# Kernel optimization log

Measured on AMD Instinct MI355X. Metric: run time of the kernel, lower is better.

## Reference

```python
import jax, jax.numpy as jnp
import numpy as np
import math

B, H, S, D = 256, 32, 16, 64
SCALE = 1.0 / math.sqrt(8.0)  # module hardcodes sqrt(8)
DROP_P = 0.3


def setup_inputs() -> dict:
    key = jax.random.key(0)
    kq, kk, kv = jax.random.split(key, 3)
    q = jax.random.normal(kq, (B, H, S, D), dtype=jnp.float32)
    k = jax.random.normal(kk, (B, H, S, D), dtype=jnp.float32)
    v = jax.random.normal(kv, (B, H, S, D), dtype=jnp.float32)
    return {"q": q, "k": k, "v": v}


def reference(q, k, v):
    # attn = (q @ k^T) / sqrt(8) + ones(16,16)
    attn = jnp.einsum("bhsd,bhtd->bhst", q, k) * SCALE
    attn = attn + jnp.ones((S, S), dtype=attn.dtype)  # additive mask (all ones)
    attn = jax.nn.softmax(attn, axis=-1)
    # dropout p=0.3 (training mode), fixed key for reproducibility
    keep = jax.random.bernoulli(jax.random.key(42), 1.0 - DROP_P, attn.shape)
    attn = jnp.where(keep, attn / (1.0 - DROP_P), 0.0)
    return jnp.einsum("bhst,bhtd->bhsd", attn, v)
```

## Files before the change

kernel.cpp:

```cpp
#include <hip/hip_runtime.h>
#include <hip/hip_bf16.h>
#include <stdint.h>
#include <stddef.h>


typedef __attribute__((ext_vector_type(8))) short short8;
typedef __attribute__((ext_vector_type(4))) float f32x4;
typedef __attribute__((ext_vector_type(4))) unsigned int u32x4;

#define VST 68
#define PST 24

__device__ __forceinline__ unsigned pk2_bf16(float a, float b) {
  float2 t; t.x = a; t.y = b;
  __hip_bfloat162 h = __float22bfloat162_rn(t);
  unsigned r;
  __builtin_memcpy(&r, &h, 4);
  return r;
}

__device__ __forceinline__ unsigned threefry_bits(unsigned idx) {
  const unsigned k0 = 0u, k1 = 42u;
  const unsigned k2 = k0 ^ k1 ^ 0x1BD11BDAu;
  unsigned x0 = k0;
  unsigned x1 = idx + k1;
#define TF_ROUND(r) { x0 += x1; x1 = (x1 << (r)) | (x1 >> (32 - (r))); x1 ^= x0; }
  TF_ROUND(13) TF_ROUND(15) TF_ROUND(26) TF_ROUND(6)
  x0 += k1; x1 += k2 + 1u;
  TF_ROUND(17) TF_ROUND(29) TF_ROUND(16) TF_ROUND(24)
  x0 += k2; x1 += k0 + 2u;
  TF_ROUND(13) TF_ROUND(15) TF_ROUND(26) TF_ROUND(6)
  x0 += k0; x1 += k1 + 3u;
  TF_ROUND(17) TF_ROUND(29) TF_ROUND(16) TF_ROUND(24)
  x0 += k1; x1 += k2 + 4u;
  TF_ROUND(13) TF_ROUND(15) TF_ROUND(26) TF_ROUND(6)
  x0 += k2; x1 += k0 + 5u;
#undef TF_ROUND
  return x0 ^ x1;
}

__device__ __forceinline__ void drop_mask(int bh, int base, float* m) {
#pragma unroll
  for (int t = 0; t < 4; t++) {
    unsigned idx = ((unsigned)bh << 8) + (unsigned)(base + t);
    unsigned bits = threefry_bits(idx);
    float u = __builtin_bit_cast(float, 0x3F800000u | (bits >> 9)) - 1.0f;
    m[t] = (u < 0.7f) ? (1.0f / 0.7f) : 0.0f;
  }
}

__device__ __forceinline__ void cvt_hilo_f4(float4 a, float4 b, short8& hi, short8& lo) {
  float x[8] = {a.x, a.y, a.z, a.w, b.x, b.y, b.z, b.w};
  u32x4 hw, lw;
#pragma unroll
  for (int i = 0; i < 4; i++) {
    float e0 = x[2 * i], e1 = x[2 * i + 1];
    unsigned hp = pk2_bf16(e0, e1);
    float h0 = __builtin_bit_cast(float, hp << 16);
    float h1 = __builtin_bit_cast(float, hp & 0xFFFF0000u);
    unsigned lp = pk2_bf16(e0 - h0, e1 - h1);
    hw[i] = hp; lw[i] = lp;
  }
  hi = __builtin_bit_cast(short8, hw);
  lo = __builtin_bit_cast(short8, lw);
}

__global__ __launch_bounds__(256, 8) void attn_kernel(
    const float* __restrict__ q, const float* __restrict__ k,
    const float* __restrict__ v, float* __restrict__ out) {
  __shared__ __align__(16) unsigned short vst[4][16 * VST];
  __shared__ __align__(16) unsigned short pst[4][16 * PST];

  const int lane = threadIdx.x & 63;
  const int w = threadIdx.x >> 6;
  const int bh = blockIdx.x * 4 + w;
  const int c = lane & 15;
  const int g = lane >> 4;

  const float4* qr = (const float4*)(q + (size_t)bh * 1024 + c * 64 + g * 8);
  const float4* kr = (const float4*)(k + (size_t)bh * 1024 + c * 64 + g * 8);
  float4 qv0 = qr[0], qv1 = qr[1], qv2 = qr[8], qv3 = qr[9];
  float4 kv0 = kr[0], kv1 = kr[1], kv2 = kr[8], kv3 = kr[9];
  const float4* vs = (const float4*)(v + (size_t)bh * 1024);
  float4 vt0 = vs[lane], vt1 = vs[64 + lane], vt2 = vs[128 + lane], vt3 = vs[192 + lane];

  float m[4];
  drop_mask(bh, (c << 4) + 4 * g, m);

  short8 qhi0, qlo0, qhi1, qlo1, khi0, klo0, khi1, klo1;
  cvt_hilo_f4(qv0, qv1, qhi0, qlo0);
  cvt_hilo_f4(qv2, qv3, qhi1, qlo1);
  cvt_hilo_f4(kv0, kv1, khi0, klo0);
  cvt_hilo_f4(kv2, kv3, khi1, klo1);

  f32x4 acc = {0.f, 0.f, 0.f, 0.f};
  acc = __builtin_amdgcn_mfma_f32_16x16x32_bf16(khi0, qhi0, acc, 0, 0, 0);
  acc = __builtin_amdgcn_mfma_f32_16x16x32_bf16(khi1, qhi1, acc, 0, 0, 0);
  acc = __builtin_amdgcn_mfma_f32_16x16x32_bf16(klo0, qhi0, acc, 0, 0, 0);
  acc = __builtin_amdgcn_mfma_f32_16x16x32_bf16(klo1, qhi1, acc, 0, 0, 0);
  acc = __builtin_amdgcn_mfma_f32_16x16x32_bf16(khi0, qlo0, acc, 0, 0, 0);
  acc = __builtin_amdgcn_mfma_f32_16x16x32_bf16(khi1, qlo1, acc, 0, 0, 0);

  const float SCALE = 0.35355339059327373f;
  float sv[4];
#pragma unroll
  for (int t = 0; t < 4; t++) sv[t] = acc[t] * SCALE;
  float mx = fmaxf(fmaxf(sv[0], sv[1]), fmaxf(sv[2], sv[3]));
  mx = fmaxf(mx, __shfl_xor(mx, 16));
  mx = fmaxf(mx, __shfl_xor(mx, 32));
  float p0 = __expf(sv[0] - mx), p1 = __expf(sv[1] - mx);
  float p2v = __expf(sv[2] - mx), p3 = __expf(sv[3] - mx);
  float sum = (p0 + p1) + (p2v + p3);
  sum += __shfl_xor(sum, 16);
  sum += __shfl_xor(sum, 32);
  float rs = 1.0f / sum;
  float ad[4] = {p0 * rs * m[0], p1 * rs * m[1], p2v * rs * m[2], p3 * rs * m[3]};

  unsigned short* vw = &vst[w][0];
  {
    float4 vv;
    unsigned w0, w1;
    vv = vt0; w0 = pk2_bf16(vv.x, vv.y); w1 = pk2_bf16(vv.z, vv.w);
    *(uint2*)(&vw[(0 + g) * VST + 4 * c]) = make_uint2(w0, w1);
    vv = vt1; w0 = pk2_bf16(vv.x, vv.y); w1 = pk2_bf16(vv.z, vv.w);
    *(uint2*)(&vw[(4 + g) * VST + 4 * c]) = make_uint2(w0, w1);
    vv = vt2; w0 = pk2_bf16(vv.x, vv.y); w1 = pk2_bf16(vv.z, vv.w);
    *(uint2*)(&vw[(8 + g) * VST + 4 * c]) = make_uint2(w0, w1);
    vv = vt3; w0 = pk2_bf16(vv.x, vv.y); w1 = pk2_bf16(vv.z, vv.w);
    *(uint2*)(&vw[(12 + g) * VST + 4 * c]) = make_uint2(w0, w1);
  }

  unsigned short* pw = &pst[w][0];
  {
    unsigned w0 = pk2_bf16(ad[0], ad[1]), w1 = pk2_bf16(ad[2], ad[3]);
    *(uint2*)(&pw[c * PST + 4 * g]) = make_uint2(w0, w1);
  }

  short8 pa = {0, 0, 0, 0, 0, 0, 0, 0};
  if (g < 2) pa = *(const short8*)(&pw[c * PST + g * 8]);

  f32x4 oacc[4];
#pragma unroll
  for (int nt = 0; nt < 4; nt++) {
    short8 vb = {0, 0, 0, 0, 0, 0, 0, 0};
    if (g < 2) {
#pragma unroll
      for (int j = 0; j < 8; j++)
        vb[j] = (short)vw[(g * 8 + j) * VST + nt * 16 + c];
    }
    f32x4 z = {0.f, 0.f, 0.f, 0.f};
    oacc[nt] = __builtin_amdgcn_mfma_f32_16x16x32_bf16(pa, vb, z, 0, 0, 0);
  }

  float* op = out + (size_t)bh * 1024;
#pragma unroll
  for (int nt = 0; nt < 4; nt++)
#pragma unroll
    for (int t = 0; t < 4; t++)
      op[(4 * g + t) * 64 + nt * 16 + c] = oacc[nt][t];
}

extern "C" void kernel_launch(void* const* d_in, const int* in_sizes, int n_in,
                              void* d_out, int out_size, void* d_ws, size_t ws_size,
                              hipStream_t stream) {
  const float* q = (const float*)d_in[0];
  const float* k = (const float*)d_in[1];
  const float* v = (const float*)d_in[2];
  float* out = (float*)d_out;
  attn_kernel<<<2048, 256, 0, stream>>>(q, k, v, out);
}
```

Before: 136.5 us.

## Process four heads per wave with register double-buffered prefetch

Each wave now loops over four consecutive batch-heads. It loads the next head's q, k, v and computes its dropout mask while working on the current head. The grid shrinks to a quarter of the blocks, and launch bounds are relaxed to allow more registers. This aims to hide global load latency through explicit prefetch, at the cost of fewer resident waves and more register pressure.

```diff
diff --git a/kernel.cpp b/kernel.cpp
--- a/kernel.cpp
+++ b/kernel.cpp
@@ -65,7 +65,7 @@
   lo = __builtin_bit_cast(short8, lw);
 }
 
-__global__ __launch_bounds__(256, 8) void attn_kernel(
+__global__ __launch_bounds__(256, 2) void attn_kernel(
     const float* __restrict__ q, const float* __restrict__ k,
     const float* __restrict__ v, float* __restrict__ out) {
   __shared__ __align__(16) unsigned short vst[4][16 * VST];
@@ -73,91 +73,115 @@
 
   const int lane = threadIdx.x & 63;
   const int w = threadIdx.x >> 6;
-  const int bh = blockIdx.x * 4 + w;
+  const int base = (blockIdx.x * 4 + w) * 4;
   const int c = lane & 15;
   const int g = lane >> 4;
 
-  const float4* qr = (const float4*)(q + (size_t)bh * 1024 + c * 64 + g * 8);
-  const float4* kr = (const float4*)(k + (size_t)bh * 1024 + c * 64 + g * 8);
-  float4 qv0 = qr[0], qv1 = qr[1], qv2 = qr[8], qv3 = qr[9];
-  float4 kv0 = kr[0], kv1 = kr[1], kv2 = kr[8], kv3 = kr[9];
-  const float4* vs = (const float4*)(v + (size_t)bh * 1024);
-  float4 vt0 = vs[lane], vt1 = vs[64 + lane], vt2 = vs[128 + lane], vt3 = vs[192 + lane];
+  float4 qv[2][4], kv[2][4], vt[2][4];
+  float m[2][4];
 
-  float m[4];
-  drop_mask(bh, (c << 4) + 4 * g, m);
-
-  short8 qhi0, qlo0, qhi1, qlo1, khi0, klo0, khi1, klo1;
-  cvt_hilo_f4(qv0, qv1, qhi0, qlo0);
-  cvt_hilo_f4(qv2, qv3, qhi1, qlo1);
-  cvt_hilo_f4(kv0, kv1, khi0, klo0);
-  cvt_hilo_f4(kv2, kv3, khi1, klo1);
-
-  f32x4 acc = {0.f, 0.f, 0.f, 0.f};
-  acc = __builtin_amdgcn_mfma_f32_16x16x32_bf16(khi0, qhi0, acc, 0, 0, 0);
-  acc = __builtin_amdgcn_mfma_f32_16x16x32_bf16(khi1, qhi1, acc, 0, 0, 0);
-  acc = __builtin_amdgcn_mfma_f32_16x16x32_bf16(klo0, qhi0, acc, 0, 0, 0);
-  acc = __builtin_amdgcn_mfma_f32_16x16x32_bf16(klo1, qhi1, acc, 0, 0, 0);
-  acc = __builtin_amdgcn_mfma_f32_16x16x32_bf16(khi0, qlo0, acc, 0, 0, 0);
-  acc = __builtin_amdgcn_mfma_f32_16x16x32_bf16(khi1, qlo1, acc, 0, 0, 0);
-
-  const float SCALE = 0.35355339059327373f;
-  float sv[4];
-#pragma unroll
-  for (int t = 0; t < 4; t++) sv[t] = acc[t] * SCALE;
-  float mx = fmaxf(fmaxf(sv[0], sv[1]), fmaxf(sv[2], sv[3]));
-  mx = fmaxf(mx, __shfl_xor(mx, 16));
-  mx = fmaxf(mx, __shfl_xor(mx, 32));
-  float p0 = __expf(sv[0] - mx), p1 = __expf(sv[1] - mx);
-  float p2v = __expf(sv[2] - mx), p3 = __expf(sv[3] - mx);
-  float sum = (p0 + p1) + (p2v + p3);
-  sum += __shfl_xor(sum, 16);
-  sum += __shfl_xor(sum, 32);
-  float rs = 1.0f / sum;
-  float ad[4] = {p0 * rs * m[0], p1 * rs * m[1], p2v * rs * m[2], p3 * rs * m[3]};
+  {
+    const float4* qr = (const float4*)(q + (size_t)base * 1024 + c * 64 + g * 8);
+    const float4* kr = (const float4*)(k + (size_t)base * 1024 + c * 64 + g * 8);
+    qv[0][0] = qr[0]; qv[0][1] = qr[1]; qv[0][2] = qr[8]; qv[0][3] = qr[9];
+    kv[0][0] = kr[0]; kv[0][1] = kr[1]; kv[0][2] = kr[8]; kv[0][3] = kr[9];
+    const float4* vs = (const float4*)(v + (size_t)base * 1024);
+    vt[0][0] = vs[lane]; vt[0][1] = vs[64 + lane];
+    vt[0][2] = vs[128 + lane]; vt[0][3] = vs[192 + lane];
+    drop_mask(base, (c << 4) + 4 * g, m[0]);
+  }
 
   unsigned short* vw = &vst[w][0];
-  {
-    float4 vv;
-    unsigned w0, w1;
-    vv = vt0; w0 = pk2_bf16(vv.x, vv.y); w1 = pk2_bf16(vv.z, vv.w);
-    *(uint2*)(&vw[(0 + g) * VST + 4 * c]) = make_uint2(w0, w1);
-    vv = vt1; w0 = pk2_bf16(vv.x, vv.y); w1 = pk2_bf16(vv.z, vv.w);
-    *(uint2*)(&vw[(4 + g) * VST + 4 * c]) = make_uint2(w0, w1);
-    vv = vt2; w0 = pk2_bf16(vv.x, vv.y); w1 = pk2_bf16(vv.z, vv.w);
-    *(uint2*)(&vw[(8 + g) * VST + 4 * c]) = make_uint2(w0, w1);
-    vv = vt3; w0 = pk2_bf16(vv.x, vv.y); w1 = pk2_bf16(vv.z, vv.w);
-    *(uint2*)(&vw[(12 + g) * VST + 4 * c]) = make_uint2(w0, w1);
+  unsigned short* pw = &pst[w][0];
+
+#pragma unroll
+  for (int h = 0; h < 4; h++) {
+    const int b = h & 1, nb = b ^ 1;
+    const int bh = base + h;
+
+    if (h < 3) {
+      const int bhn = bh + 1;
+      const float4* qr = (const float4*)(q + (size_t)bhn * 1024 + c * 64 + g * 8);
+      const float4* kr = (const float4*)(k + (size_t)bhn * 1024 + c * 64 + g * 8);
+      qv[nb][0] = qr[0]; qv[nb][1] = qr[1]; qv[nb][2] = qr[8]; qv[nb][3] = qr[9];
+      kv[nb][0] = kr[0]; kv[nb][1] = kr[1]; kv[nb][2] = kr[8]; kv[nb][3] = kr[9];
+      const float4* vs = (const float4*)(v + (size_t)bhn * 1024);
+      vt[nb][0] = vs[lane]; vt[nb][1] = vs[64 + lane];
+      vt[nb][2] = vs[128 + lane]; vt[nb][3] = vs[192 + lane];
+      drop_mask(bhn, (c << 4) + 4 * g, m[nb]);
+    }
+
+    short8 qhi0, qlo0, qhi1, qlo1, khi0, klo0, khi1, klo1;
+    cvt_hilo_f4(qv[b][0], qv[b][1], qhi0, qlo0);
+    cvt_hilo_f4(qv[b][2], qv[b][3], qhi1, qlo1);
+    cvt_hilo_f4(kv[b][0], kv[b][1], khi0, klo0);
+    cvt_hilo_f4(kv[b][2], kv[b][3], khi1, klo1);
+
+    f32x4 acc = {0.f, 0.f, 0.f, 0.f};
+    acc = __builtin_amdgcn_mfma_f32_16x16x32_bf16(khi0, qhi0, acc, 0, 0, 0);
+    acc = __builtin_amdgcn_mfma_f32_16x16x32_bf16(khi1, qhi1, acc, 0, 0, 0);
+    acc = __builtin_amdgcn_mfma_f32_16x16x32_bf16(klo0, qhi0, acc, 0, 0, 0);
+    acc = __builtin_amdgcn_mfma_f32_16x16x32_bf16(klo1, qhi1, acc, 0, 0, 0);
+    acc = __builtin_amdgcn_mfma_f32_16x16x32_bf16(khi0, qlo0, acc, 0, 0, 0);
+    acc = __builtin_amdgcn_mfma_f32_16x16x32_bf16(khi1, qlo1, acc, 0, 0, 0);
+
+    const float SCALE = 0.35355339059327373f;
+    float sv[4];
+#pragma unroll
+    for (int t = 0; t < 4; t++) sv[t] = acc[t] * SCALE;
+    float mx = fmaxf(fmaxf(sv[0], sv[1]), fmaxf(sv[2], sv[3]));
+    mx = fmaxf(mx, __shfl_xor(mx, 16));
+    mx = fmaxf(mx, __shfl_xor(mx, 32));
+    float p0 = __expf(sv[0] - mx), p1 = __expf(sv[1] - mx);
+    float p2v = __expf(sv[2] - mx), p3 = __expf(sv[3] - mx);
+    float sum = (p0 + p1) + (p2v + p3);
+    sum += __shfl_xor(sum, 16);
+    sum += __shfl_xor(sum, 32);
+    float rs = 1.0f / sum;
+    float ad[4] = {p0 * rs * m[b][0], p1 * rs * m[b][1],
+                   p2v * rs * m[b][2], p3 * rs * m[b][3]};
+
+    {
+      float4 vv;
+      unsigned w0, w1;
+      vv = vt[b][0]; w0 = pk2_bf16(vv.x, vv.y); w1 = pk2_bf16(vv.z, vv.w);
+      *(uint2*)(&vw[(0 + g) * VST + 4 * c]) = make_uint2(w0, w1);
+      vv = vt[b][1]; w0 = pk2_bf16(vv.x, vv.y); w1 = pk2_bf16(vv.z, vv.w);
+      *(uint2*)(&vw[(4 + g) * VST + 4 * c]) = make_uint2(w0, w1);
+      vv = vt[b][2]; w0 = pk2_bf16(vv.x, vv.y); w1 = pk2_bf16(vv.z, vv.w);
+      *(uint2*)(&vw[(8 + g) * VST + 4 * c]) = make_uint2(w0, w1);
+      vv = vt[b][3]; w0 = pk2_bf16(vv.x, vv.y); w1 = pk2_bf16(vv.z, vv.w);
+      *(uint2*)(&vw[(12 + g) * VST + 4 * c]) = make_uint2(w0, w1);
+    }
+
+    {
+      unsigned w0 = pk2_bf16(ad[0], ad[1]), w1 = pk2_bf16(ad[2], ad[3]);
+      *(uint2*)(&pw[c * PST + 4 * g]) = make_uint2(w0, w1);
+    }
+
+    short8 pa = {0, 0, 0, 0, 0, 0, 0, 0};
+    if (g < 2) pa = *(const short8*)(&pw[c * PST + g * 8]);
+
+    f32x4 oacc[4];
+#pragma unroll
+    for (int nt = 0; nt < 4; nt++) {
+      short8 vb = {0, 0, 0, 0, 0, 0, 0, 0};
+      if (g < 2) {
+#pragma unroll
+        for (int j = 0; j < 8; j++)
+          vb[j] = (short)vw[(g * 8 + j) * VST + nt * 16 + c];
+      }
+      f32x4 z = {0.f, 0.f, 0.f, 0.f};
+      oacc[nt] = __builtin_amdgcn_mfma_f32_16x16x32_bf16(pa, vb, z, 0, 0, 0);
+    }
+
+    float* op = out + (size_t)bh * 1024;
+#pragma unroll
+    for (int nt = 0; nt < 4; nt++)
+#pragma unroll
+      for (int t = 0; t < 4; t++)
+        op[(4 * g + t) * 64 + nt * 16 + c] = oacc[nt][t];
   }
-
-  unsigned short* pw = &pst[w][0];
-  {
-    unsigned w0 = pk2_bf16(ad[0], ad[1]), w1 = pk2_bf16(ad[2], ad[3]);
-    *(uint2*)(&pw[c * PST + 4 * g]) = make_uint2(w0, w1);
-  }
-
-  short8 pa = {0, 0, 0, 0, 0, 0, 0, 0};
-  if (g < 2) pa = *(const short8*)(&pw[c * PST + g * 8]);
-
-  f32x4 oacc[4];
-#pragma unroll
-  for (int nt = 0; nt < 4; nt++) {
-    short8 vb = {0, 0, 0, 0, 0, 0, 0, 0};
-    if (g < 2) {
-#pragma unroll
-      for (int j = 0; j < 8; j++)
-        vb[j] = (short)vw[(g * 8 + j) * VST + nt * 16 + c];
-    }
-    f32x4 z = {0.f, 0.f, 0.f, 0.f};
-    oacc[nt] = __builtin_amdgcn_mfma_f32_16x16x32_bf16(pa, vb, z, 0, 0, 0);
-  }
-
-  float* op = out + (size_t)bh * 1024;
-#pragma unroll
-  for (int nt = 0; nt < 4; nt++)
-#pragma unroll
-    for (int t = 0; t < 4; t++)
-      op[(4 * g + t) * 64 + nt * 16 + c] = oacc[nt][t];
 }
 
 extern "C" void kernel_launch(void* const* d_in, const int* in_sizes, int n_in,
@@ -167,5 +191,5 @@
   const float* k = (const float*)d_in[1];
   const float* v = (const float*)d_in[2];
   float* out = (float*)d_out;
-  attn_kernel<<<2048, 256, 0, stream>>>(q, k, v, out);
+  attn_kernel<<<512, 256, 0, stream>>>(q, k, v, out);
 }
```

Result: no change. 135.2 us (-1.0%).
